# Optimization experiments

Hardware: AMD Instinct MI355X
Metric: run time of the kernel (lower is better)

Reference implementation:

```python
import jax, jax.numpy as jnp
import numpy as np

SELECT_NUM = 5
N_OBJ = 256


def conv(x, w, b, stride=1, pad=None):
    """NCHW conv. pad=None -> VALID; pad=1 -> [(1,1),(1,1)]."""
    padding = 'VALID' if pad is None else [(pad, pad), (pad, pad)]
    out = jax.lax.conv_general_dilated(
        x, w, (stride, stride), padding,
        dimension_numbers=('NCHW', 'OIHW', 'NCHW'))
    return out + b[None, :, None, None]


def setup_inputs() -> dict:
    key = jax.random.key(0)
    ks = jax.random.split(key, 20)

    def p(k, shape, fan_in):
        return (jax.random.normal(k, shape, jnp.float32) / np.float32(np.sqrt(fan_in)))

    inp = {}
    inp['glob_feature'] = jax.random.normal(ks[0], (1, 1024, 28, 28), jnp.float32)
    inp['roi_features'] = jax.random.normal(ks[1], (N_OBJ, 2048, 7, 7), jnp.float32)
    # valid boxes in a 1280x720 image: x1>x0, y1>y0 so log(.) is finite
    x0 = jax.random.uniform(ks[2], (N_OBJ,), minval=0.0, maxval=600.0)
    y0 = jax.random.uniform(ks[3], (N_OBJ,), minval=0.0, maxval=340.0)
    x1 = x0 + jax.random.uniform(ks[4], (N_OBJ,), minval=10.0, maxval=600.0)
    y1 = y0 + jax.random.uniform(ks[5], (N_OBJ,), minval=10.0, maxval=340.0)
    inp['bbox'] = jnp.stack([x0, y0, x1, y1], axis=1)

    # global branch
    inp['w_glob1'] = p(ks[6], (512, 1024, 4, 4), 1024 * 16); inp['b_glob1'] = jnp.zeros(512, jnp.float32)
    inp['w_glob2'] = p(ks[7], (256, 512, 4, 4), 512 * 16);   inp['b_glob2'] = jnp.zeros(256, jnp.float32)
    # object branch
    inp['w_obj1'] = p(ks[8], (1024, 2048, 3, 3), 2048 * 9);  inp['b_obj1'] = jnp.zeros(1024, jnp.float32)
    inp['w_obj2'] = p(ks[9], (256, 1024, 3, 3), 1024 * 9);   inp['b_obj2'] = jnp.zeros(256, jnp.float32)
    # selector (516 = 260 obj + 256 glob)
    inp['w_sel1'] = p(ks[10], (256, 516, 3, 3), 516 * 9);    inp['b_sel1'] = jnp.zeros(256, jnp.float32)
    inp['w_sel2'] = p(ks[11], (16, 256, 3, 3), 256 * 9);     inp['b_sel2'] = jnp.zeros(16, jnp.float32)
    inp['w_sel3'] = p(ks[12], (1, 16, 3, 3), 16 * 9);        inp['b_sel3'] = jnp.zeros(1, jnp.float32)
    # FC head (eval mode: dropout = identity)
    inp['w_fc1'] = p(ks[13], (516, 256), 516);               inp['b_fc1'] = jnp.zeros(256, jnp.float32)
    inp['w_fc2'] = p(ks[14], (256 * SELECT_NUM, 64), 1280);  inp['b_fc2'] = jnp.zeros(64, jnp.float32)
    inp['w_fc3'] = p(ks[15], (64, 4), 64);                   inp['b_fc3'] = jnp.zeros(4, jnp.float32)
    return inp


def reference(glob_feature, roi_features, bbox,
              w_glob1, b_glob1, w_glob2, b_glob2,
              w_obj1, b_obj1, w_obj2, b_obj2,
              w_sel1, b_sel1, w_sel2, b_sel2, w_sel3, b_sel3,
              w_fc1, b_fc1, w_fc2, b_fc2, w_fc3, b_fc3):
    # global branch: [1,1024,28,28] -> [1,512,14,14] -> [1,256,7,7]; pool(7) is identity
    glob = jax.nn.relu(conv(glob_feature, w_glob1, b_glob1, stride=2, pad=1))
    glob = jax.nn.relu(conv(glob, w_glob2, b_glob2, stride=2, pad=1))

    # object branch: [N,2048,7,7] -> [N,1024,7,7] -> [N,256,7,7]
    obj = jax.nn.relu(conv(roi_features, w_obj1, b_obj1, pad=1))
    obj = jax.nn.relu(conv(obj, w_obj2, b_obj2, pad=1))

    # bbox normalization (uses original coords; image is 1280x720)
    x0, y0, x1, y1 = bbox[:, 0], bbox[:, 1], bbox[:, 2], bbox[:, 3]
    bb = jnp.stack([x0 / 1280.0, y0 / 720.0,
                    jnp.log(1280.0 / (x1 - x0)),
                    jnp.log(720.0 / (y1 - y0))], axis=1)  # [N,4]
    bb = jnp.broadcast_to(bb[:, :, None, None], (bb.shape[0], 4, 7, 7))
    obj = jnp.concatenate([bb, obj], axis=1)  # [N,260,7,7]

    # selector: concat with broadcast glob, 3 valid convs 7->5->3->1
    glob2 = jnp.broadcast_to(glob, (obj.shape[0], 256, 7, 7))
    s = jnp.concatenate([obj, glob2], axis=1)  # [N,516,7,7]
    s = jax.nn.relu(conv(s, w_sel1, b_sel1))
    s = jax.nn.relu(conv(s, w_sel2, b_sel2))
    s = conv(s, w_sel3, b_sel3).reshape(-1)  # [N]

    # top-k selection (sort descending over objects)
    idx = jnp.argsort(-s)[:SELECT_NUM]
    obj = obj[idx] / np.float32(SELECT_NUM)  # [5,260,7,7]

    # adaptive avg pool to 1x1 == mean over HW
    obj = obj.mean(axis=(2, 3))                               # [5,260]
    g = jnp.broadcast_to(glob.mean(axis=(2, 3)), (SELECT_NUM, 256))  # [5,256]
    x = jnp.concatenate([obj, g], axis=1)                     # [5,516]

    x = jax.nn.relu(x @ w_fc1 + b_fc1)   # dropout is identity in eval
    tmp = x.reshape(-1)                  # [1280]
    x = jax.nn.relu(tmp @ w_fc2 + b_fc2) # [64]
    x = x @ w_fc3 + b_fc3                # [4]
    return x
```

## Files before the change

kernel.cpp:

```cpp
#include <hip/hip_runtime.h>
#include <math.h>

using half8 = __attribute__((ext_vector_type(8))) _Float16;
using f32x4 = __attribute__((ext_vector_type(4))) float;

template<int CIN, int KC, int M_, int BM>
__global__ __launch_bounds__(256)
void transform_w(const float* __restrict__ w, _Float16* __restrict__ wt) {
  constexpr int NT = (KC / 32) * 9;
  __shared__ float lds[32 * 289];
  const int tid = threadIdx.x;
  const int s   = blockIdx.x;
  const int m0  = blockIdx.y * 32;
  const int ci0 = s * 32;
  int vlen = (CIN - ci0) * 9;
  if (vlen > 288) vlen = 288;
  if (vlen < 0) vlen = 0;

  for (int e = tid; e < 32 * 288; e += 256) {
    const int mi = e / 288, o = e - mi * 288;
    float v = 0.f;
    if (o < vlen) v = w[(size_t)(m0 + mi) * (CIN * 9) + (size_t)ci0 * 9 + o];
    lds[mi * 289 + o] = v;
  }
  __syncthreads();

  const int cc  = s >> 2;
  const int sub = s & 3;
  int ns = (KC - 128 * cc) / 32; if (ns > 4) ns = 4;
  const int mt = m0 / BM;
  const int mb = m0 - mt * BM;
  _Float16* base = wt + (size_t)mt * NT * (BM * 32);

  for (int u = tid; u < 36 * 256; u += 256) {
    const int chunk  = u >> 8;
    const int within = u & 255;
    const int g = chunk & 3, khkw = chunk >> 2;
    const int mi = within >> 3, i = within & 7;
    const int kt = 36 * cc + khkw * ns + sub;
    const float v = lds[mi * 289 + (8 * g + i) * 9 + khkw];
    base[(size_t)kt * (BM * 32) + g * (BM * 8) + (mb + mi) * 8 + i] = (_Float16)v;
  }
}

template<int KC, int M_, int BM, int FN, int OHW, int PAD, typename OUT_T, typename IN_T>
__global__ __launch_bounds__(512, 4)
void conv_mfma(const _Float16* __restrict__ Wt, const IN_T* __restrict__ X,
               const float* __restrict__ bias, OUT_T* __restrict__ out,
               int outc, int co_off) {
  constexpr int NT   = (KC / 32) * 9;
  constexpr int OPOS = OHW * OHW;
  constexpr int WM   = BM / 4;
  constexpr int FR   = WM / 16;

  __shared__ alignas(16) _Float16 x_s[2][50][136];

  const int tid  = threadIdx.x;
  const int wid  = tid >> 6;
  const int lane = tid & 63;
  const int g    = lane >> 4;
  const int ln   = lane & 15;
  const int obj  = wid >> 2;
  const int wm   = (wid & 3) * WM;
  const int mt   = blockIdx.x;
  const int op   = blockIdx.y;

  if (tid < 272) x_s[tid / 136][49][tid % 136] = (_Float16)0.f;

  int ohv[FN], owv[FN];
  bool pvv[FN];
#pragma unroll
  for (int f = 0; f < FN; f++) {
    const int pos = ln + 16 * f;
    pvv[f] = pos < OPOS;
    ohv[f] = pos / OHW;
    owv[f] = pos % OHW;
  }

  f32x4 acc[FR][FN];
#pragma unroll
  for (int r = 0; r < FR; r++)
#pragma unroll
    for (int f = 0; f < FN; f++) acc[r][f] = (f32x4){0.f, 0.f, 0.f, 0.f};

  const IN_T* X0 = X + (size_t)(2 * op) * KC * 49;
  const IN_T* X1 = X + (size_t)(2 * op + 1) * KC * 49;

  const _Float16* ap = Wt + (size_t)mt * NT * (BM * 32) + (g * BM + wm + ln) * 8;
  half8 afn[FR];
#pragma unroll
  for (int r = 0; r < FR; r++) afn[r] = *(const half8*)(ap + r * 128);

  for (int cbase = 0; cbase < KC; cbase += 128) {
    const int cw = (KC - cbase < 128) ? (KC - cbase) : 128;
    __syncthreads();
    for (int e = tid; e < 2 * cw * 49; e += 512) {
      const int o = e / (cw * 49);
      const int r = e - o * (cw * 49);
      const int ci = r / 49, pos = r - ci * 49;
      const float v = (float)((o ? X1 : X0)[(size_t)cbase * 49 + r]);
      x_s[o][pos][ci] = (_Float16)v;
    }
    __syncthreads();
    const int nsub = cw / 32;
    for (int khkw = 0; khkw < 9; khkw++) {
      const int kh = khkw / 3, kw = khkw - 3 * (khkw / 3);
      int boff[FN];
#pragma unroll
      for (int f = 0; f < FN; f++) {
        const int ih = ohv[f] + kh - PAD;
        const int iw = owv[f] + kw - PAD;
        bool v = pvv[f];
        if (PAD) v = v && ((unsigned)ih < 7u) && ((unsigned)iw < 7u);
        const int row = v ? (ih * 7 + iw) : 49;
        boff[f] = (obj * 50 * 136 + row * 136) * 2;
      }
      for (int sub = 0; sub < nsub; sub++) {
        half8 af[FR];
#pragma unroll
        for (int r = 0; r < FR; r++) af[r] = afn[r];
        ap += BM * 32;
#pragma unroll
        for (int r = 0; r < FR; r++)
          afn[r] = *(const half8*)(ap + r * 128);
        const char* xb = (const char*)(&x_s[0][0][0]) + (sub * 32 + 8 * g) * 2;
#pragma unroll
        for (int f = 0; f < FN; f++) {
          const half8 bf = *(const half8*)(xb + boff[f]);
#pragma unroll
          for (int r = 0; r < FR; r++)
            acc[r][f] = __builtin_amdgcn_mfma_f32_16x16x32_f16(af[r], bf, acc[r][f], 0, 0, 0);
        }
      }
    }
  }

  const int bo = 2 * op + obj;
#pragma unroll
  for (int f = 0; f < FN; f++) {
    const int pos = ln + 16 * f;
    if (pos < OPOS) {
#pragma unroll
      for (int r = 0; r < FR; r++) {
        const int mrow = wm + r * 16 + g * 4;
#pragma unroll
        for (int e = 0; e < 4; e++) {
          const int m = mt * BM + mrow + e;
          float v = acc[r][f][e] + bias[m];
          v = fmaxf(v, 0.f);
          out[((size_t)bo * outc + co_off + m) * OPOS + pos] = (OUT_T)v;
        }
      }
    }
  }
}

template<int M_, int CIN, int KH, int KW, int H, int W, int OH, int OW,
         int STRIDE, int PAD, int BATCH, int OUTC, int CO_OFF, bool RELU,
         int TM, int TN, int KSPLIT, bool PARTIAL>
__global__ __launch_bounds__(256)
void conv_gemm(const float* __restrict__ A,
               const float* __restrict__ X,
               const float* __restrict__ bias,
               float* __restrict__ out) {
  constexpr int K   = CIN * KH * KW;
  constexpr int N   = BATCH * OH * OW;
  constexpr int BK  = 16;
  constexpr int BM  = 16 * TM;
  constexpr int BN  = 16 * TN;
  constexpr int KCH = K / KSPLIT;

  __shared__ float a_s[BK][BM];
  __shared__ float b_s[BK][BN];

  const int t  = threadIdx.x;
  const int tx = t & 15;
  const int ty = t >> 4;
  const int n0 = blockIdx.x * BN;
  const int m0 = blockIdx.y * BM;
  const int kz = blockIdx.z;

  constexpr int AQ    = TM / 4;
  constexpr int TPR_A = 4 / AQ;
  const int am = t / TPR_A;
  const int ak = (t % TPR_A) * (4 * AQ);

  constexpr int BQ = TN / 4;
  const int bk = t & 15;
  const int bn = (t >> 4) * TN;

  float acc[TM][TN];
#pragma unroll
  for (int i = 0; i < TM; i++)
#pragma unroll
    for (int j = 0; j < TN; j++) acc[i][j] = 0.f;

  for (int k0 = kz * KCH; k0 < (kz + 1) * KCH; k0 += BK) {
    float4 av[AQ];
#pragma unroll
    for (int q = 0; q < AQ; q++) {
      av[q] = make_float4(0.f, 0.f, 0.f, 0.f);
      const int kq = k0 + ak + 4 * q;
      if ((m0 + am) < M_ && kq < K)
        av[q] = *reinterpret_cast<const float4*>(&A[(m0 + am) * K + kq]);
    }
    float bv[TN];
#pragma unroll
    for (int q = 0; q < TN; q++) bv[q] = 0.f;
    {
      const int kk = k0 + bk;
      if (kk < K) {
        const int ci = kk / (KH * KW);
        const int r  = kk - ci * (KH * KW);
        const int kh = r / KW;
        const int kw = r - kh * KW;
#pragma unroll
        for (int q = 0; q < TN; q++) {
          const int n = n0 + bn + q;
          if (n < N) {
            const int b   = n / (OH * OW);
            const int pos = n - b * (OH * OW);
            const int oh  = pos / OW;
            const int ow  = pos - oh * OW;
            const int ih  = oh * STRIDE - PAD + kh;
            const int iw  = ow * STRIDE - PAD + kw;
            if (ih >= 0 && ih < H && iw >= 0 && iw < W)
              bv[q] = X[((b * CIN + ci) * H + ih) * W + iw];
          }
        }
      }
    }
    __syncthreads();
#pragma unroll
    for (int q = 0; q < AQ; q++) {
      const int kq = ak + 4 * q;
      a_s[kq + 0][am] = av[q].x;
      a_s[kq + 1][am] = av[q].y;
      a_s[kq + 2][am] = av[q].z;
      a_s[kq + 3][am] = av[q].w;
    }
#pragma unroll
    for (int q = 0; q < BQ; q++)
      *reinterpret_cast<float4*>(&b_s[bk][bn + 4 * q]) =
          make_float4(bv[4 * q], bv[4 * q + 1], bv[4 * q + 2], bv[4 * q + 3]);
    __syncthreads();
#pragma unroll
    for (int kk2 = 0; kk2 < BK; kk2++) {
      float a[TM], b[TN];
#pragma unroll
      for (int q = 0; q < AQ; q++)
        *reinterpret_cast<float4*>(&a[4 * q]) =
            *reinterpret_cast<const float4*>(&a_s[kk2][ty * TM + 4 * q]);
#pragma unroll
      for (int q = 0; q < BQ; q++)
        *reinterpret_cast<float4*>(&b[4 * q]) =
            *reinterpret_cast<const float4*>(&b_s[kk2][tx * TN + 4 * q]);
#pragma unroll
      for (int i = 0; i < TM; i++)
#pragma unroll
        for (int j = 0; j < TN; j++)
          acc[i][j] = fmaf(a[i], b[j], acc[i][j]);
    }
  }

#pragma unroll
  for (int i = 0; i < TM; i++) {
    const int m = m0 + ty * TM + i;
    if (m < M_) {
#pragma unroll
      for (int j = 0; j < TN; j++) {
        const int n = n0 + tx * TN + j;
        if (n < N) {
          if (PARTIAL) {
            out[((size_t)kz * M_ + m) * N + n] = acc[i][j];
          } else {
            float v = acc[i][j] + bias[m];
            if (RELU) v = fmaxf(v, 0.f);
            const int b   = n / (OH * OW);
            const int pos = n - b * (OH * OW);
            out[(b * OUTC + CO_OFF + m) * (OH * OW) + pos] = v;
          }
        }
      }
    }
  }
}

__global__ void reduce_bias_relu(const float* __restrict__ part,
                                 const float* __restrict__ bias,
                                 float* __restrict__ out, int MN, int N, int KS) {
  const int e = blockIdx.x * 256 + threadIdx.x;
  if (e >= MN) return;
  float s = 0.f;
  for (int k = 0; k < KS; k++) s += part[(size_t)k * MN + e];
  s += bias[e / N];
  out[e] = fmaxf(s, 0.f);
}

__global__ __launch_bounds__(256)
void sel2_kernel(const float* __restrict__ x, const float* __restrict__ w,
                 const float* __restrict__ b, float* __restrict__ out) {
  const int wv   = (blockIdx.x * 256 + threadIdx.x) >> 6;
  const int lane = threadIdx.x & 63;
  const int obj  = wv >> 4, co = wv & 15;
  float acc[9];
#pragma unroll
  for (int p = 0; p < 9; p++) acc[p] = 0.f;
  const float* xo = x + (size_t)obj * 256 * 25;
  const float* wo = w + (size_t)co * 2304;
  for (int k = lane; k < 2304; k += 64) {
    const int ci = k / 9, rr = k - 9 * ci;
    const int kh = rr / 3, kw = rr - 3 * kh;
    const float wval = wo[k];
    const float* xc = xo + ci * 25;
#pragma unroll
    for (int oh = 0; oh < 3; oh++)
#pragma unroll
      for (int ow = 0; ow < 3; ow++)
        acc[oh * 3 + ow] = fmaf(xc[(oh + kh) * 5 + (ow + kw)], wval, acc[oh * 3 + ow]);
  }
  const float bv = b[co];
#pragma unroll
  for (int p = 0; p < 9; p++) {
    float v = acc[p];
#pragma unroll
    for (int off = 32; off; off >>= 1) v += __shfl_xor(v, off);
    if (lane == 0) out[(size_t)wv * 9 + p] = fmaxf(v + bv, 0.f);
  }
}

__global__ void prep_sin(const float* __restrict__ bbox,
                         const float* __restrict__ glob,
                         _Float16* __restrict__ sinb) {
  const int b = blockIdx.x;
  const float x0 = bbox[b * 4 + 0], y0 = bbox[b * 4 + 1];
  const float x1 = bbox[b * 4 + 2], y1 = bbox[b * 4 + 3];
  const float bbv[4] = {x0 / 1280.f, y0 / 720.f,
                        logf(1280.f / (x1 - x0)), logf(720.f / (y1 - y0))};
  _Float16* base = sinb + (size_t)b * 544 * 49;
  for (int e = threadIdx.x; e < 4 * 49; e += blockDim.x)
    base[e] = (_Float16)bbv[e / 49];
  for (int e = threadIdx.x; e < 256 * 49; e += blockDim.x)
    base[260 * 49 + e] = (_Float16)glob[e];
  for (int e = threadIdx.x; e < 28 * 49; e += blockDim.x)
    base[516 * 49 + e] = (_Float16)0.f;
}

__global__ void score_top5(const float* __restrict__ sel2,
                           const float* __restrict__ w3,
                           const float* __restrict__ b3,
                           int* __restrict__ idx_out) {
  __shared__ float w_s[144];
  __shared__ float s_s[256];
  const int t = threadIdx.x;
  if (t < 144) w_s[t] = w3[t];
  __syncthreads();
  float acc = b3[0];
  const float* p = sel2 + t * 144;
  for (int k = 0; k < 144; k++) acc += p[k] * w_s[k];
  s_s[t] = acc;
  __syncthreads();
  if (t == 0) {
    for (int i = 0; i < 5; i++) {
      float best = -1e30f;
      int bi = 0;
      for (int j = 0; j < 256; j++)
        if (s_s[j] > best) { best = s_s[j]; bi = j; }
      idx_out[i] = bi;
      s_s[bi] = -1e30f;
    }
  }
}

__global__ void pool_kernel(const _Float16* __restrict__ sinb,
                            const float* __restrict__ glob,
                            const int* __restrict__ idx,
                            float* __restrict__ objsel,
                            float* __restrict__ g) {
  const int blk = blockIdx.x;
  const int t = threadIdx.x;
  if (blk < 5) {
    const int b = idx[blk];
    const _Float16* base = sinb + (size_t)b * 544 * 49;
    for (int c = t; c < 260; c += blockDim.x) {
      float s = 0.f;
      for (int p = 0; p < 49; p++) s += (float)base[c * 49 + p];
      objsel[blk * 260 + c] = s * (1.f / 245.f);
    }
  } else {
    if (t < 256) {
      float s = 0.f;
      const float* p = glob + t * 49;
      for (int q = 0; q < 49; q++) s += p[q];
      g[t] = s * (1.f / 49.f);
    }
  }
}

__global__ void fc1_kernel(const float* __restrict__ objsel,
                           const float* __restrict__ g,
                           const float* __restrict__ w,
                           const float* __restrict__ b,
                           float* __restrict__ x1) {
  const int co = threadIdx.x;
  float acc[5];
#pragma unroll
  for (int i = 0; i < 5; i++) acc[i] = b[co];
  for (int k = 0; k < 260; k++) {
    const float wv = w[k * 256 + co];
#pragma unroll
    for (int i = 0; i < 5; i++) acc[i] = fmaf(objsel[i * 260 + k], wv, acc[i]);
  }
  for (int k = 260; k < 516; k++) {
    const float wv = w[k * 256 + co];
    const float gv = g[k - 260];
#pragma unroll
    for (int i = 0; i < 5; i++) acc[i] = fmaf(gv, wv, acc[i]);
  }
#pragma unroll
  for (int i = 0; i < 5; i++) x1[i * 256 + co] = fmaxf(acc[i], 0.f);
}

__global__ void fc23_kernel(const float* __restrict__ x1,
                            const float* __restrict__ w2,
                            const float* __restrict__ b2,
                            const float* __restrict__ w3,
                            const float* __restrict__ b3,
                            float* __restrict__ out) {
  __shared__ float x2[64];
  const int j = threadIdx.x;
  float acc = b2[j];
  for (int k = 0; k < 1280; k++) acc = fmaf(x1[k], w2[k * 64 + j], acc);
  x2[j] = fmaxf(acc, 0.f);
  __syncthreads();
  if (j < 4) {
    float a = b3[j];
    for (int k = 0; k < 64; k++) a = fmaf(x2[k], w3[k * 4 + j], a);
    out[j] = a;
  }
}

extern "C" void kernel_launch(void* const* d_in, const int* in_sizes, int n_in,
                              void* d_out, int out_size, void* d_ws, size_t ws_size,
                              hipStream_t stream) {
  (void)in_sizes; (void)n_in; (void)out_size; (void)ws_size;
  const float* glob_feature = (const float*)d_in[0];
  const float* roi          = (const float*)d_in[1];
  const float* bbox         = (const float*)d_in[2];
  const float* w_glob1      = (const float*)d_in[3];
  const float* b_glob1      = (const float*)d_in[4];
  const float* w_glob2      = (const float*)d_in[5];
  const float* b_glob2      = (const float*)d_in[6];
  const float* w_obj1       = (const float*)d_in[7];
  const float* b_obj1       = (const float*)d_in[8];
  const float* w_obj2       = (const float*)d_in[9];
  const float* b_obj2       = (const float*)d_in[10];
  const float* w_sel1       = (const float*)d_in[11];
  const float* b_sel1       = (const float*)d_in[12];
  const float* w_sel2       = (const float*)d_in[13];
  const float* b_sel2       = (const float*)d_in[14];
  const float* w_sel3       = (const float*)d_in[15];
  const float* b_sel3       = (const float*)d_in[16];
  const float* w_fc1        = (const float*)d_in[17];
  const float* b_fc1        = (const float*)d_in[18];
  const float* w_fc2        = (const float*)d_in[19];
  const float* b_fc2        = (const float*)d_in[20];
  const float* w_fc3        = (const float*)d_in[21];
  const float* b_fc3        = (const float*)d_in[22];

  float* ws = (float*)d_ws;
  _Float16* wbuf1   = (_Float16*)(ws);
  _Float16* sinbuf  = (_Float16*)(ws);
  _Float16* wbuf2   = (_Float16*)(ws + 3412000);
  _Float16* wbufs1  = (_Float16*)(ws + 4591648);
  float*    sel1buf = ws + 5218336;
  float*    glob1buf= ws + 6856736;
  float*    part1   = ws + 6957088;
  float*    part2   = ws + 8562720;
  float*    sel2buf = ws + 8763424;
  _Float16* obj1buf = (_Float16*)(ws + 9437184);
  float*    globbuf = ws + 15859712;
  int*      idxbuf  = (int*)(ws + 15872256);
  float*    objsel  = ws + 15872264;
  float*    gbuf    = ws + 15873564;
  float*    x1buf   = ws + 15873820;

  transform_w<2048, 2048, 1024, 256><<<dim3(64, 32), 256, 0, stream>>>(w_obj1, wbuf1);
  conv_mfma<2048, 1024, 256, 4, 7, 1, _Float16, float>
      <<<dim3(4, 128), 512, 0, stream>>>(wbuf1, roi, b_obj1, obj1buf, 1024, 0);

  transform_w<1024, 1024, 256, 128><<<dim3(32, 8), 256, 0, stream>>>(w_obj2, wbuf2);
  transform_w<516, 544, 256, 128><<<dim3(17, 8), 256, 0, stream>>>(w_sel1, wbufs1);

  conv_gemm<512, 1024, 4, 4, 28, 28, 14, 14, 2, 1, 1, 512, 0, true, 4, 4, 16, true>
      <<<dim3(4, 8, 16), 256, 0, stream>>>(w_glob1, glob_feature, b_glob1, part1);
  reduce_bias_relu<<<dim3(392), 256, 0, stream>>>(part1, b_glob1, glob1buf, 100352, 196, 16);
  conv_gemm<256, 512, 4, 4, 14, 14, 7, 7, 2, 1, 1, 256, 0, true, 4, 4, 16, true>
      <<<dim3(1, 4, 16), 256, 0, stream>>>(w_glob2, glob1buf, b_glob2, part2);
  reduce_bias_relu<<<dim3(49), 256, 0, stream>>>(part2, b_glob2, globbuf, 12544, 49, 16);

  prep_sin<<<dim3(256), 256, 0, stream>>>(bbox, globbuf, sinbuf);

  conv_mfma<1024, 256, 128, 4, 7, 1, _Float16, _Float16>
      <<<dim3(2, 128), 512, 0, stream>>>(wbuf2, obj1buf, b_obj2, sinbuf, 544, 4);
  conv_mfma<544, 256, 128, 2, 5, 0, float, _Float16>
      <<<dim3(2, 128), 512, 0, stream>>>(wbufs1, sinbuf, b_sel1, sel1buf, 256, 0);
  sel2_kernel<<<dim3(1024), 256, 0, stream>>>(sel1buf, w_sel2, b_sel2, sel2buf);
  score_top5<<<dim3(1), 256, 0, stream>>>(sel2buf, w_sel3, b_sel3, idxbuf);

  pool_kernel<<<dim3(6), 256, 0, stream>>>(sinbuf, globbuf, idxbuf, objsel, gbuf);
  fc1_kernel<<<dim3(1), 256, 0, stream>>>(objsel, gbuf, w_fc1, b_fc1, x1buf);
  fc23_kernel<<<dim3(1), 64, 0, stream>>>(x1buf, w_fc2, b_fc2, w_fc3, b_fc3,
                                          (float*)d_out);
}
```

Measured before the change: 1.140 ms.

## Switch conv activations to channel-last fp16 with vectorized prefetched LDS loads

A new transpose-convert pass turns the ROI features into position-major fp16 rows. The intermediate object and selector buffers are stored the same way, using vectorized half4 epilogue stores. conv_mfma now fills its LDS tiles with 16-byte vector loads and prefetches the next channel chunk into registers while the current one is computed. This replaces the old scalar, division-heavy strided gather and transpose into shared memory. The cost is an extra full conversion pass over the ROI tensor and a larger workspace, and the fast path only runs when ws_size is at least 115 MB.

```diff
diff --git a/kernel.cpp b/kernel.cpp
--- a/kernel.cpp
+++ b/kernel.cpp
@@ -2,6 +2,7 @@
 #include <math.h>
 
 using half8 = __attribute__((ext_vector_type(8))) _Float16;
+using half4 = __attribute__((ext_vector_type(4))) _Float16;
 using f32x4 = __attribute__((ext_vector_type(4))) float;
 
 template<int CIN, int KC, int M_, int BM>
@@ -43,7 +44,27 @@
   }
 }
 
-template<int KC, int M_, int BM, int FN, int OHW, int PAD, typename OUT_T, typename IN_T>
+__global__ __launch_bounds__(256)
+void convert_tr(const float* __restrict__ x, _Float16* __restrict__ xh) {
+  __shared__ _Float16 t_s[49][136];
+  const int tid   = threadIdx.x;
+  const int cbase = blockIdx.x * 128;
+  const int obj   = blockIdx.y;
+  const float* src = x + (size_t)obj * 2048 * 49 + (size_t)cbase * 49;
+  for (int e = tid; e < 128 * 49; e += 256) {
+    const int ci = e / 49, pos = e - ci * 49;
+    t_s[pos][ci] = (_Float16)src[e];
+  }
+  __syncthreads();
+  _Float16* dst = xh + (size_t)obj * 49 * 2048 + cbase;
+  for (int u = tid; u < 49 * 16; u += 256) {
+    const int pos = u >> 4, l = u & 15;
+    *(half8*)&dst[(size_t)pos * 2048 + l * 8] = *(const half8*)&t_s[pos][l * 8];
+  }
+}
+
+template<int KC, int M_, int BM, int FN, int OHW, int PAD, bool TIN, int XROW,
+         bool TOUT, typename OUT_T, typename IN_T>
 __global__ __launch_bounds__(512, 4)
 void conv_mfma(const _Float16* __restrict__ Wt, const IN_T* __restrict__ X,
                const float* __restrict__ bias, OUT_T* __restrict__ out,
@@ -83,23 +104,73 @@
 #pragma unroll
     for (int f = 0; f < FN; f++) acc[r][f] = (f32x4){0.f, 0.f, 0.f, 0.f};
 
-  const IN_T* X0 = X + (size_t)(2 * op) * KC * 49;
-  const IN_T* X1 = X + (size_t)(2 * op + 1) * KC * 49;
+  const _Float16* Xh = nullptr;
+  if constexpr (TIN) Xh = (const _Float16*)X + (size_t)(2 * op) * 49 * XROW;
+
+  half8 rg[4];
+  auto load_chunk = [&](int cbase, int cw) {
+    if (cw == 128) {
+#pragma unroll
+      for (int v = 0; v < 4; v++) {
+        const int u = v * 512 + tid;
+        if (u < 1568) {
+          const int row = u >> 4, l = u & 15;
+          const int o = row >= 49 ? 1 : 0, pos = row - 49 * o;
+          rg[v] = *(const half8*)(Xh + (size_t)(o * 49 + pos) * XROW + cbase + l * 8);
+        }
+      }
+    } else {
+      if (tid < 392) {
+        const int row = tid >> 2, l = tid & 3;
+        const int o = row >= 49 ? 1 : 0, pos = row - 49 * o;
+        rg[0] = *(const half8*)(Xh + (size_t)(o * 49 + pos) * XROW + cbase + l * 8);
+      }
+    }
+  };
+  auto write_chunk = [&](int cw) {
+    if (cw == 128) {
+#pragma unroll
+      for (int v = 0; v < 4; v++) {
+        const int u = v * 512 + tid;
+        if (u < 1568) {
+          const int row = u >> 4, l = u & 15;
+          const int o = row >= 49 ? 1 : 0, pos = row - 49 * o;
+          *(half8*)&x_s[o][pos][l * 8] = rg[v];
+        }
+      }
+    } else {
+      if (tid < 392) {
+        const int row = tid >> 2, l = tid & 3;
+        const int o = row >= 49 ? 1 : 0, pos = row - 49 * o;
+        *(half8*)&x_s[o][pos][l * 8] = rg[0];
+      }
+    }
+  };
 
   const _Float16* ap = Wt + (size_t)mt * NT * (BM * 32) + (g * BM + wm + ln) * 8;
   half8 afn[FR];
 #pragma unroll
   for (int r = 0; r < FR; r++) afn[r] = *(const half8*)(ap + r * 128);
+
+  if constexpr (TIN) load_chunk(0, KC < 128 ? KC : 128);
 
   for (int cbase = 0; cbase < KC; cbase += 128) {
     const int cw = (KC - cbase < 128) ? (KC - cbase) : 128;
     __syncthreads();
-    for (int e = tid; e < 2 * cw * 49; e += 512) {
-      const int o = e / (cw * 49);
-      const int r = e - o * (cw * 49);
-      const int ci = r / 49, pos = r - ci * 49;
-      const float v = (float)((o ? X1 : X0)[(size_t)cbase * 49 + r]);
-      x_s[o][pos][ci] = (_Float16)v;
+    if constexpr (TIN) {
+      write_chunk(cw);
+      if (cbase + 128 < KC) {
+        const int nw = (KC - cbase - 128 < 128) ? (KC - cbase - 128) : 128;
+        load_chunk(cbase + 128, nw);
+      }
+    } else {
+      for (int e = tid; e < 2 * cw * 49; e += 512) {
+        const int o = e / (cw * 49);
+        const int r = e - o * (cw * 49);
+        const int ci = r / 49, pos = r - ci * 49;
+        const float v = (float)(X[(size_t)(2 * op + o) * KC * 49 + (size_t)cbase * 49 + r]);
+        x_s[o][pos][ci] = (_Float16)v;
+      }
     }
     __syncthreads();
     const int nsub = cw / 32;
@@ -142,13 +213,20 @@
     if (pos < OPOS) {
 #pragma unroll
       for (int r = 0; r < FR; r++) {
-        const int mrow = wm + r * 16 + g * 4;
-#pragma unroll
-        for (int e = 0; e < 4; e++) {
-          const int m = mt * BM + mrow + e;
-          float v = acc[r][f][e] + bias[m];
-          v = fmaxf(v, 0.f);
-          out[((size_t)bo * outc + co_off + m) * OPOS + pos] = (OUT_T)v;
+        const int mrow = mt * BM + wm + r * 16 + g * 4;
+        if constexpr (TOUT) {
+          half4 h;
+#pragma unroll
+          for (int e = 0; e < 4; e++)
+            h[e] = (_Float16)fmaxf(acc[r][f][e] + bias[mrow + e], 0.f);
+          *(half4*)&((_Float16*)out)[((size_t)bo * OPOS + pos) * outc + co_off + mrow] = h;
+        } else {
+#pragma unroll
+          for (int e = 0; e < 4; e++) {
+            const int m = mrow + e;
+            float v = fmaxf(acc[r][f][e] + bias[m], 0.f);
+            out[((size_t)bo * outc + co_off + m) * OPOS + pos] = (OUT_T)v;
+          }
         }
       }
     }
@@ -329,21 +407,23 @@
   }
 }
 
-__global__ void prep_sin(const float* __restrict__ bbox,
-                         const float* __restrict__ glob,
-                         _Float16* __restrict__ sinb) {
+__global__ void prep_sin_t(const float* __restrict__ bbox,
+                           const float* __restrict__ glob,
+                           _Float16* __restrict__ sint) {
   const int b = blockIdx.x;
   const float x0 = bbox[b * 4 + 0], y0 = bbox[b * 4 + 1];
   const float x1 = bbox[b * 4 + 2], y1 = bbox[b * 4 + 3];
   const float bbv[4] = {x0 / 1280.f, y0 / 720.f,
                         logf(1280.f / (x1 - x0)), logf(720.f / (y1 - y0))};
-  _Float16* base = sinb + (size_t)b * 544 * 49;
-  for (int e = threadIdx.x; e < 4 * 49; e += blockDim.x)
-    base[e] = (_Float16)bbv[e / 49];
-  for (int e = threadIdx.x; e < 256 * 49; e += blockDim.x)
-    base[260 * 49 + e] = (_Float16)glob[e];
-  for (int e = threadIdx.x; e < 28 * 49; e += blockDim.x)
-    base[516 * 49 + e] = (_Float16)0.f;
+  _Float16* base = sint + (size_t)b * 49 * 544;
+  for (int e = threadIdx.x; e < 49 * 288; e += blockDim.x) {
+    const int pos = e / 288, q = e - pos * 288;
+    float v; int c;
+    if (q < 4)        { v = bbv[q];                  c = q; }
+    else if (q < 260) { v = glob[(q - 4) * 49 + pos]; c = q + 256; }
+    else              { v = 0.f;                      c = q + 256; }
+    base[pos * 544 + c] = (_Float16)v;
+  }
 }
 
 __global__ void score_top5(const float* __restrict__ sel2,
@@ -372,19 +452,19 @@
   }
 }
 
-__global__ void pool_kernel(const _Float16* __restrict__ sinb,
-                            const float* __restrict__ glob,
-                            const int* __restrict__ idx,
-                            float* __restrict__ objsel,
-                            float* __restrict__ g) {
+__global__ void pool_t(const _Float16* __restrict__ sint,
+                       const float* __restrict__ glob,
+                       const int* __restrict__ idx,
+                       float* __restrict__ objsel,
+                       float* __restrict__ g) {
   const int blk = blockIdx.x;
   const int t = threadIdx.x;
   if (blk < 5) {
     const int b = idx[blk];
-    const _Float16* base = sinb + (size_t)b * 544 * 49;
+    const _Float16* base = sint + (size_t)b * 49 * 544;
     for (int c = t; c < 260; c += blockDim.x) {
       float s = 0.f;
-      for (int p = 0; p < 49; p++) s += (float)base[c * 49 + p];
+      for (int p = 0; p < 49; p++) s += (float)base[p * 544 + c];
       objsel[blk * 260 + c] = s * (1.f / 245.f);
     }
   } else {
@@ -443,7 +523,7 @@
 extern "C" void kernel_launch(void* const* d_in, const int* in_sizes, int n_in,
                               void* d_out, int out_size, void* d_ws, size_t ws_size,
                               hipStream_t stream) {
-  (void)in_sizes; (void)n_in; (void)out_size; (void)ws_size;
+  (void)in_sizes; (void)n_in; (void)out_size;
   const float* glob_feature = (const float*)d_in[0];
   const float* roi          = (const float*)d_in[1];
   const float* bbox         = (const float*)d_in[2];
@@ -469,25 +549,57 @@
   const float* b_fc3        = (const float*)d_in[22];
 
   float* ws = (float*)d_ws;
-  _Float16* wbuf1   = (_Float16*)(ws);
-  _Float16* sinbuf  = (_Float16*)(ws);
-  _Float16* wbuf2   = (_Float16*)(ws + 3412000);
-  _Float16* wbufs1  = (_Float16*)(ws + 4591648);
-  float*    sel1buf = ws + 5218336;
-  float*    glob1buf= ws + 6856736;
-  float*    part1   = ws + 6957088;
-  float*    part2   = ws + 8562720;
-  float*    sel2buf = ws + 8763424;
-  _Float16* obj1buf = (_Float16*)(ws + 9437184);
-  float*    globbuf = ws + 15859712;
-  int*      idxbuf  = (int*)(ws + 15872256);
-  float*    objsel  = ws + 15872264;
-  float*    gbuf    = ws + 15873564;
-  float*    x1buf   = ws + 15873820;
+  const bool big = ws_size >= (size_t)115000000;
+
+  _Float16 *xh1, *wbuf1, *obj1buf, *sint, *wbuf2, *wbufs1;
+  float *sel1buf, *glob1buf, *part1, *part2, *sel2buf, *globbuf, *objsel, *gbuf, *x1buf;
+  int* idxbuf;
+
+  if (big) {
+    xh1      = (_Float16*)(ws);
+    wbuf1    = (_Float16*)(ws + 12845056);
+    obj1buf  = (_Float16*)(ws + 22282240);
+    sint     = (_Float16*)(ws);
+    wbuf2    = (_Float16*)(ws + 3411968);
+    wbufs1   = (_Float16*)(ws + 4591616);
+    sel1buf  = ws + 5218304;
+    glob1buf = ws + 6856704;
+    part1    = ws + 6957056;
+    part2    = ws + 8562688;
+    sel2buf  = ws + 8763392;
+    globbuf  = ws + 8800256;
+    idxbuf   = (int*)(ws + 8812800);
+    objsel   = ws + 8812808;
+    gbuf     = ws + 8814108;
+    x1buf    = ws + 8814364;
+  } else {
+    xh1      = nullptr;
+    wbuf1    = (_Float16*)(ws);
+    sint     = (_Float16*)(ws);
+    wbuf2    = (_Float16*)(ws + 3412000);
+    wbufs1   = (_Float16*)(ws + 4591648);
+    sel1buf  = ws + 5218336;
+    glob1buf = ws + 6856736;
+    part1    = ws + 6957088;
+    part2    = ws + 8562720;
+    sel2buf  = ws + 8763424;
+    obj1buf  = (_Float16*)(ws + 9437184);
+    globbuf  = ws + 15859712;
+    idxbuf   = (int*)(ws + 15872256);
+    objsel   = ws + 15872264;
+    gbuf     = ws + 15873564;
+    x1buf    = ws + 15873820;
+  }
 
   transform_w<2048, 2048, 1024, 256><<<dim3(64, 32), 256, 0, stream>>>(w_obj1, wbuf1);
-  conv_mfma<2048, 1024, 256, 4, 7, 1, _Float16, float>
-      <<<dim3(4, 128), 512, 0, stream>>>(wbuf1, roi, b_obj1, obj1buf, 1024, 0);
+  if (big) {
+    convert_tr<<<dim3(16, 256), 256, 0, stream>>>(roi, xh1);
+    conv_mfma<2048, 1024, 256, 4, 7, 1, true, 2048, true, _Float16, _Float16>
+        <<<dim3(4, 128), 512, 0, stream>>>(wbuf1, xh1, b_obj1, obj1buf, 1024, 0);
+  } else {
+    conv_mfma<2048, 1024, 256, 4, 7, 1, false, 0, true, _Float16, float>
+        <<<dim3(4, 128), 512, 0, stream>>>(wbuf1, roi, b_obj1, obj1buf, 1024, 0);
+  }
 
   transform_w<1024, 1024, 256, 128><<<dim3(32, 8), 256, 0, stream>>>(w_obj2, wbuf2);
   transform_w<516, 544, 256, 128><<<dim3(17, 8), 256, 0, stream>>>(w_sel1, wbufs1);
@@ -499,16 +611,16 @@
       <<<dim3(1, 4, 16), 256, 0, stream>>>(w_glob2, glob1buf, b_glob2, part2);
   reduce_bias_relu<<<dim3(49), 256, 0, stream>>>(part2, b_glob2, globbuf, 12544, 49, 16);
 
-  prep_sin<<<dim3(256), 256, 0, stream>>>(bbox, globbuf, sinbuf);
-
-  conv_mfma<1024, 256, 128, 4, 7, 1, _Float16, _Float16>
-      <<<dim3(2, 128), 512, 0, stream>>>(wbuf2, obj1buf, b_obj2, sinbuf, 544, 4);
-  conv_mfma<544, 256, 128, 2, 5, 0, float, _Float16>
-      <<<dim3(2, 128), 512, 0, stream>>>(wbufs1, sinbuf, b_sel1, sel1buf, 256, 0);
+  prep_sin_t<<<dim3(256), 256, 0, stream>>>(bbox, globbuf, sint);
+
+  conv_mfma<1024, 256, 128, 4, 7, 1, true, 1024, true, _Float16, _Float16>
+      <<<dim3(2, 128), 512, 0, stream>>>(wbuf2, obj1buf, b_obj2, sint, 544, 4);
+  conv_mfma<544, 256, 128, 2, 5, 0, true, 544, false, float, _Float16>
+      <<<dim3(2, 128), 512, 0, stream>>>(wbufs1, sint, b_sel1, sel1buf, 256, 0);
   sel2_kernel<<<dim3(1024), 256, 0, stream>>>(sel1buf, w_sel2, b_sel2, sel2buf);
   score_top5<<<dim3(1), 256, 0, stream>>>(sel2buf, w_sel3, b_sel3, idxbuf);
 
-  pool_kernel<<<dim3(6), 256, 0, stream>>>(sinbuf, globbuf, idxbuf, objsel, gbuf);
+  pool_t<<<dim3(6), 256, 0, stream>>>(sint, globbuf, idxbuf, objsel, gbuf);
   fc1_kernel<<<dim3(1), 256, 0, stream>>>(objsel, gbuf, w_fc1, b_fc1, x1buf);
   fc23_kernel<<<dim3(1), 64, 0, stream>>>(x1buf, w_fc2, b_fc2, w_fc3, b_fc3,
                                           (float*)d_out);
```

New measurement: 1.154 ms. No clear change (+1.2%).
